# Performance work log

Hardware: AMD Instinct MI355X
Metric: run time of the kernel (lower is better)

Reference implementation:

```python
import jax, jax.numpy as jnp
import numpy as np

N_NODES = 100000
N_EDGES = 3200000
D_FEAT = 64


def setup_inputs() -> dict:
    key = jax.random.key(0)
    k1, k2, k3 = jax.random.split(key, 3)
    x = jax.random.normal(k1, (N_NODES, D_FEAT), dtype=jnp.float32)
    up_index = jax.random.randint(k2, (2, N_EDGES), 0, N_NODES, dtype=jnp.int64)
    down_index = jax.random.randint(k3, (2, N_EDGES), 0, N_NODES, dtype=jnp.int64)
    return {"x": x, "up_index": up_index, "down_index": down_index}


def _propagate(x, edge_index, num_nodes):
    # flow = 'source_to_target': (i, j) = (1, 0)
    # __lift__: gather x along node_dim=-2 at source indices (row j=0)
    msg = x[edge_index[0]]                      # [E, D]  message_up(x_j) = x_j
    # aggregate 'add': scatter-add messages to target indices (row i=1)
    return jax.ops.segment_sum(msg, edge_index[1], num_segments=num_nodes)  # [N, D]


def reference(x, up_index, down_index):
    up_out = _propagate(x, up_index, x.shape[0])
    down_out = _propagate(x, down_index, x.shape[0])
    # update: combine up and down aggregations (identity update -> sum)
    return up_out + down_out
```

## Files before the change

### kernel.cpp

```cpp
#include <hip/hip_runtime.h>


static constexpr int D = 64;
static constexpr int Q = 16;
static constexpr int NPB = 64;
static constexpr int NPB_SHIFT = 6;
static constexpr int CHUNK = 8192;
static constexpr int CH = 4096;
static constexpr int MAXT = 32;

__global__ void detect_idx_dtype(const int* __restrict__ w, int* __restrict__ flag) {
    int tid = threadIdx.x;
    int v = w[2 * tid + 1];
    unsigned long long m = __ballot(v != 0);
    if (tid == 0) *flag = (m == 0ULL) ? 1 : 0;
}

__device__ __forceinline__ int load_idx_nt(const void* idx, long long i, int is64) {
    return is64 ? (int)__builtin_nontemporal_load(((const long long*)idx) + i)
                : __builtin_nontemporal_load(((const int*)idx) + i);
}

__global__ __launch_bounds__(256) void bucket_hist_kernel(
        const void* __restrict__ up, const void* __restrict__ down,
        int* __restrict__ bcounts, const int* __restrict__ flag, int E, int NB) {
    extern __shared__ int lcnt[];
    const int is64 = *flag;
    for (int i = threadIdx.x; i < NB; i += blockDim.x) lcnt[i] = 0;
    __syncthreads();
    const long long total = 2LL * E;
    const long long stride = (long long)gridDim.x * blockDim.x;
    for (long long e = (long long)blockIdx.x * blockDim.x + threadIdx.x;
         e < total; e += stride) {
        const void* idx = up; long long ee = e;
        if (ee >= E) { idx = down; ee -= E; }
        int dst = load_idx_nt(idx, E + ee, is64);
        atomicAdd(&lcnt[dst >> NPB_SHIFT], 1);
    }
    __syncthreads();
    for (int i = threadIdx.x; i < NB; i += blockDim.x)
        if (lcnt[i]) atomicAdd(&bcounts[i], lcnt[i]);
}

__global__ __launch_bounds__(1024) void scan_kernel(
        const int* __restrict__ counts, int* __restrict__ offsets,
        int* __restrict__ cursors, int NB) {
    __shared__ int sums[1024];
    const int tid = threadIdx.x;
    const int chunk = (NB + 1023) / 1024;
    const int start = tid * chunk;
    const int end = min(start + chunk, NB);
    int s = 0;
    for (int i = start; i < end; i++) s += counts[i];
    sums[tid] = s;
    __syncthreads();
    for (int off = 1; off < 1024; off <<= 1) {
        int t = (tid >= off) ? sums[tid - off] : 0;
        __syncthreads();
        sums[tid] += t;
        __syncthreads();
    }
    int run = (tid == 0) ? 0 : sums[tid - 1];
    for (int i = start; i < end; i++) {
        offsets[i] = run;
        cursors[i] = run;
        run += counts[i];
    }
    if (tid == 1023) offsets[NB] = run;
}

__global__ __launch_bounds__(512) void bucket_scatter_kernel(
        const void* __restrict__ up, const void* __restrict__ down,
        int* __restrict__ gcursor, unsigned* __restrict__ packed,
        const int* __restrict__ flag, int E, int NB) {
    extern __shared__ int lds[];
    int* cnt = lds;
    int* base = lds + NB;
    const int is64 = *flag;
    const long long total = 2LL * E;
    const long long cs = (long long)blockIdx.x * CHUNK;
    if (cs >= total) return;
    const int m = (int)(min(total, cs + (long long)CHUNK) - cs);
    const int tid = threadIdx.x;

    for (int i = tid; i < NB; i += 512) cnt[i] = 0;
    __syncthreads();

    unsigned pr[16];
    int bkt[16];
    #pragma unroll
    for (int k = 0; k < 16; k++) {
        const int i = tid + (k << 9);
        bkt[k] = -1;
        if (i < m) {
            long long e = cs + i;
            const void* idx = up; long long ee = e;
            if (ee >= E) { idx = down; ee -= E; }
            const int src = load_idx_nt(idx, ee, is64);
            const int dst = load_idx_nt(idx, E + ee, is64);
            pr[k] = ((unsigned)src << NPB_SHIFT) | (unsigned)(dst & (NPB - 1));
            bkt[k] = dst >> NPB_SHIFT;
            atomicAdd(&cnt[bkt[k]], 1);
        }
    }
    __syncthreads();
    for (int i = tid; i < NB; i += 512) {
        int c = cnt[i];
        base[i] = c ? atomicAdd(&gcursor[i], c) : 0;
        cnt[i] = 0;
    }
    __syncthreads();
    #pragma unroll
    for (int k = 0; k < 16; k++) {
        if (bkt[k] >= 0) {
            int pos = base[bkt[k]] + atomicAdd(&cnt[bkt[k]], 1);
            packed[pos] = pr[k];
        }
    }
}

__global__ __launch_bounds__(256) void bucket_gather_kernel(
        const float* __restrict__ x, const int* __restrict__ offsets,
        const unsigned* __restrict__ packed, float* __restrict__ out,
        int N, int shift, int NT) {
    extern __shared__ int lds[];
    unsigned* sorted = (unsigned*)lds;
    int* cnt = lds + CH;
    int* binoff = cnt + NT * NPB;
    const int nbins = NT * NPB;

    const int b = blockIdx.x;
    const int tid = threadIdx.x;
    const int g = tid >> 4;
    const int q = tid & 15;
    const int beg = offsets[b], end = offsets[b + 1];
    const float* xq = x + q * 4;

    float4 acc0 = make_float4(0.f, 0.f, 0.f, 0.f);
    float4 acc1 = acc0, acc2 = acc0, acc3 = acc0;

#define LOAD1(E) (*(const float4*)(xq + ((long long)(sorted[E] >> NPB_SHIFT)) * D))
#define DRAIN(A, E, RE) do {                                                   \
        for (; (E) + 4 <= (RE); (E) += 4) {                                    \
            const float4 w0 = LOAD1((E) + 0), w1 = LOAD1((E) + 1);             \
            const float4 w2 = LOAD1((E) + 2), w3 = LOAD1((E) + 3);             \
            A.x += (w0.x + w1.x) + (w2.x + w3.x);                              \
            A.y += (w0.y + w1.y) + (w2.y + w3.y);                              \
            A.z += (w0.z + w1.z) + (w2.z + w3.z);                              \
            A.w += (w0.w + w1.w) + (w2.w + w3.w);                              \
        }                                                                      \
        for (; (E) < (RE); (E)++) {                                            \
            const float4 w = LOAD1(E);                                         \
            A.x += w.x; A.y += w.y; A.z += w.z; A.w += w.w;                    \
        }                                                                      \
    } while (0)

    for (int cs = beg; cs < end; cs += CH) {
        const int m = min(CH, end - cs);
        for (int i = tid; i < nbins; i += 256) cnt[i] = 0;
        __syncthreads();
        unsigned pr[16];
        #pragma unroll
        for (int k = 0; k < 16; k++) {
            const int i = tid + (k << 8);
            if (i < m) {
                unsigned p = __builtin_nontemporal_load(packed + cs + i);
                pr[k] = p;
                int key = (int)((p >> (NPB_SHIFT + shift)) << NPB_SHIFT) | (int)(p & (NPB - 1));
                atomicAdd(&cnt[key], 1);
            }
        }
        __syncthreads();
        if (tid < 64) {
            const int K = (nbins + 63) >> 6;
            const int base = tid * K;
            int S = 0;
            for (int k = 0; k < K; k++) {
                int i = base + k;
                if (i < nbins) S += cnt[i];
            }
            int inc = S;
            #pragma unroll
            for (int off = 1; off < 64; off <<= 1) {
                int t = __shfl_up(inc, off, 64);
                if (tid >= off) inc += t;
            }
            int run = inc - S;
            for (int k = 0; k < K; k++) {
                int i = base + k;
                if (i < nbins) {
                    int c = cnt[i];
                    cnt[i] = run;
                    binoff[i + 1] = run + c;
                    run += c;
                }
            }
            if (tid == 0) binoff[0] = 0;
        }
        __syncthreads();
        #pragma unroll
        for (int k = 0; k < 16; k++) {
            const int i = tid + (k << 8);
            if (i < m) {
                unsigned p = pr[k];
                int key = (int)((p >> (NPB_SHIFT + shift)) << NPB_SHIFT) | (int)(p & (NPB - 1));
                int pos = atomicAdd(&cnt[key], 1);
                sorted[pos] = p;
            }
        }
        __syncthreads();

        for (int t = 0; t < NT; t++) {
            const int kb = t * NPB + 4 * g;
            const int c0 = binoff[kb], c1 = binoff[kb + 1], c2 = binoff[kb + 2];
            const int c3 = binoff[kb + 3], c4 = binoff[kb + 4];
            int e0 = c0, e1 = c1, e2 = c2, e3 = c3;
            while (e0 + 2 <= c1 && e1 + 2 <= c2 && e2 + 2 <= c3 && e3 + 2 <= c4) {
                const float4 u0 = LOAD1(e0), u1 = LOAD1(e0 + 1);
                const float4 u2 = LOAD1(e1), u3 = LOAD1(e1 + 1);
                const float4 u4 = LOAD1(e2), u5 = LOAD1(e2 + 1);
                const float4 u6 = LOAD1(e3), u7 = LOAD1(e3 + 1);
                acc0.x += u0.x + u1.x; acc0.y += u0.y + u1.y;
                acc0.z += u0.z + u1.z; acc0.w += u0.w + u1.w;
                acc1.x += u2.x + u3.x; acc1.y += u2.y + u3.y;
                acc1.z += u2.z + u3.z; acc1.w += u2.w + u3.w;
                acc2.x += u4.x + u5.x; acc2.y += u4.y + u5.y;
                acc2.z += u4.z + u5.z; acc2.w += u4.w + u5.w;
                acc3.x += u6.x + u7.x; acc3.y += u6.y + u7.y;
                acc3.z += u6.z + u7.z; acc3.w += u6.w + u7.w;
                e0 += 2; e1 += 2; e2 += 2; e3 += 2;
            }
            DRAIN(acc0, e0, c1);
            DRAIN(acc1, e1, c2);
            DRAIN(acc2, e2, c3);
            DRAIN(acc3, e3, c4);
        }
        __syncthreads();
    }
#undef DRAIN
#undef LOAD1

    const int node0 = b * NPB + 4 * g;
    if (node0 < N)
        *(float4*)(out + (long long)node0 * D + q * 4) = acc0;
    if (node0 + 1 < N)
        *(float4*)(out + (long long)(node0 + 1) * D + q * 4) = acc1;
    if (node0 + 2 < N)
        *(float4*)(out + (long long)(node0 + 2) * D + q * 4) = acc2;
    if (node0 + 3 < N)
        *(float4*)(out + (long long)(node0 + 3) * D + q * 4) = acc3;
}

__global__ __launch_bounds__(256) void scatter_add_kernel(
        const float* __restrict__ x, const void* __restrict__ up_idx,
        const void* __restrict__ down_idx, float* __restrict__ out,
        const int* __restrict__ dtype_flag, int num_edges) {
    const int is64 = *dtype_flag;
    const long long total = 2LL * num_edges * Q;
    const long long stride = (long long)gridDim.x * blockDim.x;
    for (long long t = (long long)blockIdx.x * blockDim.x + threadIdx.x;
         t < total; t += stride) {
        const int quad = (int)(t & (Q - 1));
        long long eg = t >> 4;
        const void* idx = up_idx;
        if (eg >= num_edges) { idx = down_idx; eg -= num_edges; }
        int src = load_idx_nt(idx, eg, is64);
        int dst = load_idx_nt(idx, num_edges + eg, is64);
        const float4 v = *(const float4*)(x + (long long)src * D + quad * 4);
        float* o = out + (long long)dst * D + quad * 4;
        unsafeAtomicAdd(o + 0, v.x);
        unsafeAtomicAdd(o + 1, v.y);
        unsafeAtomicAdd(o + 2, v.z);
        unsafeAtomicAdd(o + 3, v.w);
    }
}

extern "C" void kernel_launch(void* const* d_in, const int* in_sizes, int n_in,
                              void* d_out, int out_size, void* d_ws, size_t ws_size,
                              hipStream_t stream) {
    const float* x = (const float*)d_in[0];
    const void* up_idx = d_in[1];
    const void* down_idx = d_in[2];
    float* out = (float*)d_out;

    const int E = in_sizes[1] / 2;
    const int N = out_size / D;
    const int NB = (N + NPB - 1) / NPB;
    const long long Etot = 2LL * E;

    int shift = 13;
    while ((((long long)(N - 1) >> shift) + 1) > MAXT) shift++;
    const int NT = (int)(((long long)(N - 1) >> shift) + 1);

    int* ws_i = (int*)d_ws;
    int* flag = ws_i;
    int* counts = ws_i + 64;
    int* offsets = counts + NB;
    int* cursors = offsets + NB + 15;
    unsigned* packed = (unsigned*)(cursors + NB);
    const size_t ws_need = (size_t)(64 + 3LL * NB + 16 + Etot) * 4 + 64;

    detect_idx_dtype<<<1, 64, 0, stream>>>((const int*)up_idx, flag);

    if (ws_size >= ws_need && N <= (1 << 25) && Etot < (1LL << 31)) {
        hipMemsetAsync(counts, 0, (size_t)NB * sizeof(int), stream);
        bucket_hist_kernel<<<2048, 256, NB * sizeof(int), stream>>>(
            up_idx, down_idx, counts, flag, E, NB);
        scan_kernel<<<1, 1024, 0, stream>>>(counts, offsets, cursors, NB);
        const int sblocks = (int)((Etot + CHUNK - 1) / CHUNK);
        bucket_scatter_kernel<<<sblocks, 512, 2 * NB * sizeof(int), stream>>>(
            up_idx, down_idx, cursors, packed, flag, E, NB);
        const int nbins = NT * NPB;
        const size_t glds = (size_t)(CH + 2 * nbins + 4) * 4;
        bucket_gather_kernel<<<NB, 256, glds, stream>>>(
            x, offsets, packed, out, N, shift, NT);
    } else {
        hipMemsetAsync(d_out, 0, (size_t)out_size * sizeof(float), stream);
        scatter_add_kernel<<<8192, 256, 0, stream>>>(x, up_idx, down_idx, out, flag, E);
    }
}
```

Measured before the change: 482.2 us.

## Split each node's edges across four wavefront slots and reduce with shuffles

The gather kernel's work mapping changes. Before, each 16-lane group owned four consecutive nodes and walked their edge lists serially. Now each 64-lane wavefront owns 16 nodes and processes each node's edges four at a time across its four 16-lane slots, then combines the partial sums with cross-lane shuffles. This is meant to even out load imbalance from varying node degrees and keep more loads in flight. In exchange it adds 16 float4 accumulators per thread, which raises register pressure, plus masked tail iterations and shuffle reductions.

```diff
diff --git a/kernel.cpp b/kernel.cpp
--- a/kernel.cpp
+++ b/kernel.cpp
@@ -131,29 +131,16 @@
 
     const int b = blockIdx.x;
     const int tid = threadIdx.x;
-    const int g = tid >> 4;
-    const int q = tid & 15;
+    const int w = tid >> 6;
+    const int lane = tid & 63;
+    const int slot = lane >> 4;
+    const int q = lane & 15;
     const int beg = offsets[b], end = offsets[b + 1];
     const float* xq = x + q * 4;
 
-    float4 acc0 = make_float4(0.f, 0.f, 0.f, 0.f);
-    float4 acc1 = acc0, acc2 = acc0, acc3 = acc0;
-
-#define LOAD1(E) (*(const float4*)(xq + ((long long)(sorted[E] >> NPB_SHIFT)) * D))
-#define DRAIN(A, E, RE) do {                                                   \
-        for (; (E) + 4 <= (RE); (E) += 4) {                                    \
-            const float4 w0 = LOAD1((E) + 0), w1 = LOAD1((E) + 1);             \
-            const float4 w2 = LOAD1((E) + 2), w3 = LOAD1((E) + 3);             \
-            A.x += (w0.x + w1.x) + (w2.x + w3.x);                              \
-            A.y += (w0.y + w1.y) + (w2.y + w3.y);                              \
-            A.z += (w0.z + w1.z) + (w2.z + w3.z);                              \
-            A.w += (w0.w + w1.w) + (w2.w + w3.w);                              \
-        }                                                                      \
-        for (; (E) < (RE); (E)++) {                                            \
-            const float4 w = LOAD1(E);                                         \
-            A.x += w.x; A.y += w.y; A.z += w.z; A.w += w.w;                    \
-        }                                                                      \
-    } while (0)
+    float4 acc[16];
+    #pragma unroll
+    for (int j = 0; j < 16; j++) acc[j] = make_float4(0.f, 0.f, 0.f, 0.f);
 
     for (int cs = beg; cs < end; cs += CH) {
         const int m = min(CH, end - cs);
@@ -211,44 +198,38 @@
         __syncthreads();
 
         for (int t = 0; t < NT; t++) {
-            const int kb = t * NPB + 4 * g;
-            const int c0 = binoff[kb], c1 = binoff[kb + 1], c2 = binoff[kb + 2];
-            const int c3 = binoff[kb + 3], c4 = binoff[kb + 4];
-            int e0 = c0, e1 = c1, e2 = c2, e3 = c3;
-            while (e0 + 2 <= c1 && e1 + 2 <= c2 && e2 + 2 <= c3 && e3 + 2 <= c4) {
-                const float4 u0 = LOAD1(e0), u1 = LOAD1(e0 + 1);
-                const float4 u2 = LOAD1(e1), u3 = LOAD1(e1 + 1);
-                const float4 u4 = LOAD1(e2), u5 = LOAD1(e2 + 1);
-                const float4 u6 = LOAD1(e3), u7 = LOAD1(e3 + 1);
-                acc0.x += u0.x + u1.x; acc0.y += u0.y + u1.y;
-                acc0.z += u0.z + u1.z; acc0.w += u0.w + u1.w;
-                acc1.x += u2.x + u3.x; acc1.y += u2.y + u3.y;
-                acc1.z += u2.z + u3.z; acc1.w += u2.w + u3.w;
-                acc2.x += u4.x + u5.x; acc2.y += u4.y + u5.y;
-                acc2.z += u4.z + u5.z; acc2.w += u4.w + u5.w;
-                acc3.x += u6.x + u7.x; acc3.y += u6.y + u7.y;
-                acc3.z += u6.z + u7.z; acc3.w += u6.w + u7.w;
-                e0 += 2; e1 += 2; e2 += 2; e3 += 2;
-            }
-            DRAIN(acc0, e0, c1);
-            DRAIN(acc1, e1, c2);
-            DRAIN(acc2, e2, c3);
-            DRAIN(acc3, e3, c4);
-        }
-        __syncthreads();
-    }
-#undef DRAIN
-#undef LOAD1
-
-    const int node0 = b * NPB + 4 * g;
-    if (node0 < N)
-        *(float4*)(out + (long long)node0 * D + q * 4) = acc0;
-    if (node0 + 1 < N)
-        *(float4*)(out + (long long)(node0 + 1) * D + q * 4) = acc1;
-    if (node0 + 2 < N)
-        *(float4*)(out + (long long)(node0 + 2) * D + q * 4) = acc2;
-    if (node0 + 3 < N)
-        *(float4*)(out + (long long)(node0 + 3) * D + q * 4) = acc3;
+            const int kb = t * NPB + 16 * w;
+            #pragma unroll
+            for (int j = 0; j < 16; j++) {
+                const int rb = binoff[kb + j];
+                const int re = binoff[kb + j + 1];
+                for (int e = rb; e < re; e += 4) {
+                    const int idx = e + slot;
+                    const unsigned p = sorted[min(idx, re - 1)];
+                    const float4 v = *(const float4*)(xq + ((long long)(p >> NPB_SHIFT)) * D);
+                    const bool act = idx < re;
+                    acc[j].x += act ? v.x : 0.f;
+                    acc[j].y += act ? v.y : 0.f;
+                    acc[j].z += act ? v.z : 0.f;
+                    acc[j].w += act ? v.w : 0.f;
+                }
+            }
+        }
+        __syncthreads();
+    }
+
+    const int node0 = b * NPB + 16 * w;
+    #pragma unroll
+    for (int j = 0; j < 16; j++) {
+        float4 a = acc[j];
+        a.x += __shfl_xor(a.x, 16, 64); a.y += __shfl_xor(a.y, 16, 64);
+        a.z += __shfl_xor(a.z, 16, 64); a.w += __shfl_xor(a.w, 16, 64);
+        a.x += __shfl_xor(a.x, 32, 64); a.y += __shfl_xor(a.y, 32, 64);
+        a.z += __shfl_xor(a.z, 32, 64); a.w += __shfl_xor(a.w, 32, 64);
+        const int node = node0 + j;
+        if (slot == 0 && node < N)
+            *(float4*)(out + (long long)node * D + q * 4) = a;
+    }
 }
 
 __global__ __launch_bounds__(256) void scatter_add_kernel(
```

After: 581.2 us. 1.21x slower.
